# Optimization experiments

Measured on AMD Instinct MI355X. Metric: run time of the kernel, lower is better.

Reference implementation:

```python
import jax, jax.numpy as jnp
import numpy as np
from jax import lax

V, B, T, H = 16, 64, 256, 128  # num_variables, batch, seq_len, rnn_hidden_size
FC, C = 256, 10                # fc_hidden_size, num_classes


def setup_inputs() -> dict:
    key = jax.random.key(0)
    ks = jax.random.split(key, 8)
    s = 1.0 / np.sqrt(H)
    return {
        "x":   jax.random.normal(ks[0], (V, B, T, 1), jnp.float32),
        "Wih": jax.random.uniform(ks[1], (V, 3 * H, 1), jnp.float32, -s, s),
        "Whh": jax.random.uniform(ks[2], (V, 3 * H, H), jnp.float32, -s, s),
        "bih": jnp.zeros((V, 3 * H), jnp.float32),
        "bhh": jnp.zeros((V, 3 * H), jnp.float32),
        "Wp":  jax.random.normal(ks[3], (V, H), jnp.float32) * s,  # xavier-ish
        "bp":  jnp.zeros((V,), jnp.float32),
        "W1":  jax.random.normal(ks[4], (FC, V), jnp.float32) * (1.0 / np.sqrt(V)),
        "b1":  jnp.zeros((FC,), jnp.float32),
        "W2":  jax.random.normal(ks[5], (C, FC), jnp.float32) * (1.0 / np.sqrt(FC)),
        "b2":  jnp.zeros((C,), jnp.float32),
    }


def reference(x, Wih, Whh, bih, bhh, Wp, bp, W1, b1, W2, b2):
    # Batched multi-head GRU: all V independent heads scanned together.
    # Precompute input-side gates for all steps: [T, V, B, 3H]
    gi = jnp.einsum('vbti,vgi->tvbg', x, Wih) + bih[None, :, None, :]

    def step(h, gi_t):
        gh = jnp.einsum('vbh,vgh->vbg', h, Whh) + bhh[:, None, :]
        i_r, i_z, i_n = jnp.split(gi_t, 3, axis=-1)
        h_r, h_z, h_n = jnp.split(gh, 3, axis=-1)
        r = jax.nn.sigmoid(i_r + h_r)
        z = jax.nn.sigmoid(i_z + h_z)
        n = jnp.tanh(i_n + r * h_n)
        h_new = (1.0 - z) * n + z * h  # PyTorch GRU update
        return h_new, None

    h0 = jnp.zeros((x.shape[0], x.shape[1], Whh.shape[-1]), x.dtype)
    h_last, _ = lax.scan(step, h0, gi)  # [V, B, H] — last timestep hidden

    # per-variable Linear(H, 1), then concat over variables -> [B, V]
    concat = jnp.einsum('vbh,vh->bv', h_last, Wp) + bp[None, :]

    # Classifier: Linear -> ReLU -> Linear
    hfc = jax.nn.relu(concat @ W1.T + b1)
    return hfc @ W2.T + b2  # [B, C]
```

## Files before the change

### kernel.cpp

```cpp
#include <hip/hip_runtime.h>

#define NV  16
#define NB  64
#define NT  256
#define NH  128
#define NFC 256
#define NC  10

typedef _Float16 half8  __attribute__((ext_vector_type(8)));
typedef _Float16 half4t __attribute__((ext_vector_type(4)));
typedef float    f32x4  __attribute__((ext_vector_type(4)));

__global__ __launch_bounds__(512, 2) void gru_scan_kernel(
    const float* __restrict__ x,   const float* __restrict__ Wih,
    const float* __restrict__ Whh, const float* __restrict__ bih,
    const float* __restrict__ bhh, const float* __restrict__ Wp,
    const float* __restrict__ bp,  float* __restrict__ concat_ws)
{
    __shared__ __align__(16) _Float16 frag[2][2048];
    __shared__ float xT[NT][17];
    __shared__ float pc[8][16];

    const int tid = threadIdx.x;
    const int w   = tid >> 6;
    const int l   = tid & 63;
    const int r   = l & 15;
    const int m4  = l >> 4;
    const int bid = blockIdx.x;
    const int v   = bid >> 2;
    const int b0  = (bid & 3) << 4;
    const int j0  = (w << 4) + (m4 << 2);

    constexpr float L2E = 1.44269504088896340736f;
    const float SCL0 = -L2E, SCL1 = -L2E, SCL2 = 2.0f * L2E;

    {
        const int rr = tid >> 5;
        const int t0 = (tid & 31) << 3;
        const float* xp = x + ((size_t)(v * NB + b0 + rr) * NT + t0);
        float4 a = *(const float4*)xp;
        float4 b = *(const float4*)(xp + 4);
        xT[t0+0][rr] = a.x; xT[t0+1][rr] = a.y; xT[t0+2][rr] = a.z; xT[t0+3][rr] = a.w;
        xT[t0+4][rr] = b.x; xT[t0+5][rr] = b.y; xT[t0+6][rr] = b.z; xT[t0+7][rr] = b.w;
    }
    ((unsigned long long*)(&frag[0][0]))[tid] = 0ull;

    half8 afr[3][4];
    #pragma unroll
    for (int g = 0; g < 3; ++g) {
        const float s = (g == 2) ? SCL2 : SCL0;
        #pragma unroll
        for (int kb = 0; kb < 4; ++kb) {
            const float* wpp = Whh + (size_t)(v * 384 + g * 128 + (w << 4) + r) * 128
                             + kb * 32 + m4 * 8;
            float4 lo = *(const float4*)wpp;
            float4 hi = *(const float4*)(wpp + 4);
            half8 hf;
            hf[0]=(_Float16)(s*lo.x); hf[1]=(_Float16)(s*lo.y);
            hf[2]=(_Float16)(s*lo.z); hf[3]=(_Float16)(s*lo.w);
            hf[4]=(_Float16)(s*hi.x); hf[5]=(_Float16)(s*hi.y);
            hf[6]=(_Float16)(s*hi.z); hf[7]=(_Float16)(s*hi.w);
            afr[g][kb] = hf;
        }
    }

    float wihs_[3][4], bihs_[3][4];
    f32x4 c0i, c1i, c2i;
    #pragma unroll
    for (int g = 0; g < 3; ++g) {
        const float s = (g == 2) ? SCL2 : SCL0;
        #pragma unroll
        for (int q = 0; q < 4; ++q) {
            const int idx = v * 384 + g * 128 + j0 + q;
            wihs_[g][q] = s * Wih[idx];
            bihs_[g][q] = s * bih[idx];
            const float bs = s * bhh[idx];
            if (g == 0) c0i[q] = bs; else if (g == 1) c1i[q] = bs; else c2i[q] = bs;
        }
    }
    float wpv[4];
    #pragma unroll
    for (int q = 0; q < 4; ++q) wpv[q] = Wp[v * NH + j0 + q];

    float h_old[4] = {0.f, 0.f, 0.f, 0.f};

    const int sub8  = (j0 & 31) >> 3;
    const int fwoff = (j0 >> 5) * 512 + (r + 16 * sub8) * 8 + (j0 & 7);
    const int rdoff = l * 8;

    __syncthreads();

    auto step = [&](const _Float16* __restrict__ fb, _Float16* __restrict__ fwb,
                    const float xr) {
        half8 bfr[4];
        #pragma unroll
        for (int kb = 0; kb < 4; ++kb)
            bfr[kb] = *(const half8*)(fb + kb * 512 + rdoff);

        f32x4 acc0 = __builtin_amdgcn_mfma_f32_16x16x32_f16(afr[0][0], bfr[0], c0i, 0, 0, 0);
        f32x4 acc1 = __builtin_amdgcn_mfma_f32_16x16x32_f16(afr[1][0], bfr[0], c1i, 0, 0, 0);
        f32x4 acc2 = __builtin_amdgcn_mfma_f32_16x16x32_f16(afr[2][0], bfr[0], c2i, 0, 0, 0);
        #pragma unroll
        for (int kb = 1; kb < 4; ++kb) {
            acc0 = __builtin_amdgcn_mfma_f32_16x16x32_f16(afr[0][kb], bfr[kb], acc0, 0, 0, 0);
            acc1 = __builtin_amdgcn_mfma_f32_16x16x32_f16(afr[1][kb], bfr[kb], acc1, 0, 0, 0);
            acc2 = __builtin_amdgcn_mfma_f32_16x16x32_f16(afr[2][kb], bfr[kb], acc2, 0, 0, 0);
        }

        float rg[4], av[4];
        #pragma unroll
        for (int q = 0; q < 4; ++q) {
            const float srs = fmaf(xr, wihs_[0][q], bihs_[0][q]) + acc0[q];
            const float szs = fmaf(xr, wihs_[1][q], bihs_[1][q]) + acc1[q];
            rg[q] = __builtin_amdgcn_rcpf(1.f + __builtin_amdgcn_exp2f(srs));
            av[q] = __builtin_amdgcn_exp2f(szs);
        }
        half4t hv;
        #pragma unroll
        for (int q = 0; q < 4; ++q) {
            const float gns = fmaf(xr, wihs_[2][q], bihs_[2][q]);
            const float ccs = fmaf(rg[q], acc2[q], gns);
            const float b   = __builtin_amdgcn_exp2f(-ccs);
            const float a   = av[q];
            const float h   = h_old[q];
            const float num = fmaf(-a, b, a) + fmaf(h, b, h);
            const float den = (1.f + a) * (1.f + b);
            const float hn  = num * __builtin_amdgcn_rcpf(den);
            h_old[q] = hn;
            hv[q] = (_Float16)hn;
        }
        *(half4t*)(fwb + fwoff) = hv;
        __syncthreads();
    };

    for (int t = 0; t < NT; t += 2) {
        const float xa = xT[t][r];
        const float xb = xT[t + 1][r];
        step(&frag[0][0], &frag[1][0], xa);
        step(&frag[1][0], &frag[0][0], xb);
    }

    float partial = h_old[0]*wpv[0] + h_old[1]*wpv[1] + h_old[2]*wpv[2] + h_old[3]*wpv[3];
    partial += __shfl_xor(partial, 16, 64);
    partial += __shfl_xor(partial, 32, 64);
    if (l < 16) pc[w][l] = partial;
    __syncthreads();
    if (tid < 16) {
        float s = bp[v];
        #pragma unroll
        for (int ww = 0; ww < 8; ++ww) s += pc[ww][tid];
        concat_ws[(b0 + tid) * NV + v] = s;
    }
}

__global__ __launch_bounds__(256, 1) void fc_kernel(
    const float* __restrict__ cws, const float* __restrict__ W1,
    const float* __restrict__ b1,  const float* __restrict__ W2,
    const float* __restrict__ b2,  float* __restrict__ out)
{
    __shared__ float cc[NB][NV + 1];
    __shared__ float hfc[NB][NFC + 1];
    const int tid = threadIdx.x;
    for (int i = tid; i < NB * NV; i += 256) cc[i >> 4][i & 15] = cws[i];
    __syncthreads();

    float w1r[NV];
    #pragma unroll
    for (int q = 0; q < NV; q += 4) {
        float4 t4 = *(const float4*)(W1 + tid * NV + q);
        w1r[q] = t4.x; w1r[q+1] = t4.y; w1r[q+2] = t4.z; w1r[q+3] = t4.w;
    }
    const float bb = b1[tid];
    for (int b = 0; b < NB; ++b) {
        float s = bb;
        #pragma unroll
        for (int q = 0; q < NV; ++q) s = fmaf(cc[b][q], w1r[q], s);
        hfc[b][tid] = fmaxf(s, 0.f);
    }
    __syncthreads();

    for (int idx = tid; idx < NB * NC; idx += 256) {
        const int b = idx / NC, c = idx % NC;
        const float* w2r = W2 + c * NFC;
        float s = b2[c];
        #pragma unroll 4
        for (int f = 0; f < NFC; f += 4) {
            float4 wv = *(const float4*)(w2r + f);
            s = fmaf(hfc[b][f+0], wv.x, s);
            s = fmaf(hfc[b][f+1], wv.y, s);
            s = fmaf(hfc[b][f+2], wv.z, s);
            s = fmaf(hfc[b][f+3], wv.w, s);
        }
        out[idx] = s;
    }
}

extern "C" void kernel_launch(void* const* d_in, const int* in_sizes, int n_in,
                              void* d_out, int out_size, void* d_ws, size_t ws_size,
                              hipStream_t stream) {
    const float* x   = (const float*)d_in[0];
    const float* Wih = (const float*)d_in[1];
    const float* Whh = (const float*)d_in[2];
    const float* bih = (const float*)d_in[3];
    const float* bhh = (const float*)d_in[4];
    const float* Wp  = (const float*)d_in[5];
    const float* bp  = (const float*)d_in[6];
    const float* W1  = (const float*)d_in[7];
    const float* b1  = (const float*)d_in[8];
    const float* W2  = (const float*)d_in[9];
    const float* b2  = (const float*)d_in[10];
    float* out = (float*)d_out;
    float* cws = (float*)d_ws;

    gru_scan_kernel<<<dim3(64), dim3(512), 0, stream>>>(x, Wih, Whh, bih, bhh, Wp, bp, cws);
    fc_kernel<<<dim3(1), dim3(256), 0, stream>>>(cws, W1, b1, W2, b2, out);
}
```

Measured before the change: 240.9 us.

## Split batch into 4-row tiles across 256 blocks with shuffle-based gate redistribution

Each GRU block now handles 4 batch rows instead of 16, so the launch grows from 64 to 256 blocks and uses more compute units for the sequential scan. The MFMA still runs at 16-wide N, so 12 of its 16 columns hold zero padding. Lanes use cross-lane shuffles to pick out their own gate value, so each thread does the elementwise work for one hidden unit instead of four. This shortens the per-step elementwise critical path and spreads the latency-bound recurrence over more CUs. The cost is wasted MFMA throughput and extra shuffles every step.

```diff
diff --git a/kernel.cpp b/kernel.cpp
--- a/kernel.cpp
+++ b/kernel.cpp
@@ -8,7 +8,6 @@
 #define NC  10
 
 typedef _Float16 half8  __attribute__((ext_vector_type(8)));
-typedef _Float16 half4t __attribute__((ext_vector_type(4)));
 typedef float    f32x4  __attribute__((ext_vector_type(4)));
 
 __global__ __launch_bounds__(512, 2) void gru_scan_kernel(
@@ -18,37 +17,41 @@
     const float* __restrict__ bp,  float* __restrict__ concat_ws)
 {
     __shared__ __align__(16) _Float16 frag[2][2048];
-    __shared__ float xT[NT][17];
-    __shared__ float pc[8][16];
+    __shared__ float xT[NT][5];
+    __shared__ float pc[8][4];
 
     const int tid = threadIdx.x;
     const int w   = tid >> 6;
     const int l   = tid & 63;
     const int r   = l & 15;
     const int m4  = l >> 4;
+    const int rb  = r & 3;
+    const int s   = r >> 2;
     const int bid = blockIdx.x;
-    const int v   = bid >> 2;
-    const int b0  = (bid & 3) << 4;
+    const int v   = bid >> 4;
+    const int b0  = (bid & 15) << 2;
     const int j0  = (w << 4) + (m4 << 2);
+    const int j   = j0 + s;
 
     constexpr float L2E = 1.44269504088896340736f;
-    const float SCL0 = -L2E, SCL1 = -L2E, SCL2 = 2.0f * L2E;
+    const float SCL0 = -L2E, SCL2 = 2.0f * L2E;
 
     {
-        const int rr = tid >> 5;
-        const int t0 = (tid & 31) << 3;
-        const float* xp = x + ((size_t)(v * NB + b0 + rr) * NT + t0);
-        float4 a = *(const float4*)xp;
-        float4 b = *(const float4*)(xp + 4);
-        xT[t0+0][rr] = a.x; xT[t0+1][rr] = a.y; xT[t0+2][rr] = a.z; xT[t0+3][rr] = a.w;
-        xT[t0+4][rr] = b.x; xT[t0+5][rr] = b.y; xT[t0+6][rr] = b.z; xT[t0+7][rr] = b.w;
-    }
-    ((unsigned long long*)(&frag[0][0]))[tid] = 0ull;
+        const int rr = tid >> 7;
+        const int t0 = (tid & 127) << 1;
+        const float2 xv = *(const float2*)(x + (size_t)(v * NB + b0 + rr) * NT + t0);
+        xT[t0][rr] = xv.x; xT[t0 + 1][rr] = xv.y;
+    }
+    {
+        unsigned* fz = (unsigned*)frag;
+        #pragma unroll
+        for (int i = 0; i < 4; ++i) fz[tid + i * 512] = 0u;
+    }
 
     half8 afr[3][4];
     #pragma unroll
     for (int g = 0; g < 3; ++g) {
-        const float s = (g == 2) ? SCL2 : SCL0;
+        const float sc = (g == 2) ? SCL2 : SCL0;
         #pragma unroll
         for (int kb = 0; kb < 4; ++kb) {
             const float* wpp = Whh + (size_t)(v * 384 + g * 128 + (w << 4) + r) * 128
@@ -56,36 +59,33 @@
             float4 lo = *(const float4*)wpp;
             float4 hi = *(const float4*)(wpp + 4);
             half8 hf;
-            hf[0]=(_Float16)(s*lo.x); hf[1]=(_Float16)(s*lo.y);
-            hf[2]=(_Float16)(s*lo.z); hf[3]=(_Float16)(s*lo.w);
-            hf[4]=(_Float16)(s*hi.x); hf[5]=(_Float16)(s*hi.y);
-            hf[6]=(_Float16)(s*hi.z); hf[7]=(_Float16)(s*hi.w);
+            hf[0]=(_Float16)(sc*lo.x); hf[1]=(_Float16)(sc*lo.y);
+            hf[2]=(_Float16)(sc*lo.z); hf[3]=(_Float16)(sc*lo.w);
+            hf[4]=(_Float16)(sc*hi.x); hf[5]=(_Float16)(sc*hi.y);
+            hf[6]=(_Float16)(sc*hi.z); hf[7]=(_Float16)(sc*hi.w);
             afr[g][kb] = hf;
         }
     }
 
-    float wihs_[3][4], bihs_[3][4];
     f32x4 c0i, c1i, c2i;
     #pragma unroll
+    for (int q = 0; q < 4; ++q) {
+        c0i[q] = SCL0 * bhh[v * 384 +   0 + j0 + q];
+        c1i[q] = SCL0 * bhh[v * 384 + 128 + j0 + q];
+        c2i[q] = SCL2 * bhh[v * 384 + 256 + j0 + q];
+    }
+    float wihs_[3], bihs_[3];
+    #pragma unroll
     for (int g = 0; g < 3; ++g) {
-        const float s = (g == 2) ? SCL2 : SCL0;
-        #pragma unroll
-        for (int q = 0; q < 4; ++q) {
-            const int idx = v * 384 + g * 128 + j0 + q;
-            wihs_[g][q] = s * Wih[idx];
-            bihs_[g][q] = s * bih[idx];
-            const float bs = s * bhh[idx];
-            if (g == 0) c0i[q] = bs; else if (g == 1) c1i[q] = bs; else c2i[q] = bs;
-        }
-    }
-    float wpv[4];
-    #pragma unroll
-    for (int q = 0; q < 4; ++q) wpv[q] = Wp[v * NH + j0 + q];
-
-    float h_old[4] = {0.f, 0.f, 0.f, 0.f};
-
-    const int sub8  = (j0 & 31) >> 3;
-    const int fwoff = (j0 >> 5) * 512 + (r + 16 * sub8) * 8 + (j0 & 7);
+        const float sc = (g == 2) ? SCL2 : SCL0;
+        wihs_[g] = sc * Wih[v * 384 + g * 128 + j];
+        bihs_[g] = sc * bih[v * 384 + g * 128 + j];
+    }
+    const float wpj = Wp[v * NH + j];
+
+    float h_old = 0.f;
+
+    const int fwoff = (j >> 5) * 512 + (rb + 16 * ((j & 31) >> 3)) * 8 + (j & 7);
     const int rdoff = l * 8;
 
     __syncthreads();
@@ -107,49 +107,54 @@
             acc2 = __builtin_amdgcn_mfma_f32_16x16x32_f16(afr[2][kb], bfr[kb], acc2, 0, 0, 0);
         }
 
-        float rg[4], av[4];
-        #pragma unroll
-        for (int q = 0; q < 4; ++q) {
-            const float srs = fmaf(xr, wihs_[0][q], bihs_[0][q]) + acc0[q];
-            const float szs = fmaf(xr, wihs_[1][q], bihs_[1][q]) + acc1[q];
-            rg[q] = __builtin_amdgcn_rcpf(1.f + __builtin_amdgcn_exp2f(srs));
-            av[q] = __builtin_amdgcn_exp2f(szs);
-        }
-        half4t hv;
-        #pragma unroll
-        for (int q = 0; q < 4; ++q) {
-            const float gns = fmaf(xr, wihs_[2][q], bihs_[2][q]);
-            const float ccs = fmaf(rg[q], acc2[q], gns);
-            const float b   = __builtin_amdgcn_exp2f(-ccs);
-            const float a   = av[q];
-            const float h   = h_old[q];
-            const float num = fmaf(-a, b, a) + fmaf(h, b, h);
-            const float den = (1.f + a) * (1.f + b);
-            const float hn  = num * __builtin_amdgcn_rcpf(den);
-            h_old[q] = hn;
-            hv[q] = (_Float16)hn;
-        }
-        *(half4t*)(fwb + fwoff) = hv;
+        const bool sel1 = (s & 1) != 0, sel2 = (s & 2) != 0;
+        float gv[3];
+        #pragma unroll
+        for (int g = 0; g < 3; ++g) {
+            const f32x4& a4 = (g == 0) ? acc0 : (g == 1) ? acc1 : acc2;
+            const float t4  = __shfl_xor(a4[1], 4, 64);
+            const float t8  = __shfl_xor(a4[2], 8, 64);
+            const float t12 = __shfl_xor(a4[3], 12, 64);
+            const float lo  = sel1 ? t4  : a4[0];
+            const float hi  = sel1 ? t12 : t8;
+            gv[g] = sel2 ? hi : lo;
+        }
+
+        const float srs = fmaf(xr, wihs_[0], bihs_[0]) + gv[0];
+        const float szs = fmaf(xr, wihs_[1], bihs_[1]) + gv[1];
+        const float gns = fmaf(xr, wihs_[2], bihs_[2]);
+        const float rg  = __builtin_amdgcn_rcpf(1.f + __builtin_amdgcn_exp2f(srs));
+        const float a   = __builtin_amdgcn_exp2f(szs);
+        const float ccs = fmaf(rg, gv[2], gns);
+        const float b   = __builtin_amdgcn_exp2f(-ccs);
+        const float h   = h_old;
+        const float num = fmaf(-a, b, a) + fmaf(h, b, h);
+        const float den = (1.f + a) * (1.f + b);
+        const float hn  = num * __builtin_amdgcn_rcpf(den);
+        h_old = hn;
+        fwb[fwoff] = (_Float16)hn;
         __syncthreads();
     };
 
     for (int t = 0; t < NT; t += 2) {
-        const float xa = xT[t][r];
-        const float xb = xT[t + 1][r];
+        const float xa = xT[t][rb];
+        const float xb = xT[t + 1][rb];
         step(&frag[0][0], &frag[1][0], xa);
         step(&frag[1][0], &frag[0][0], xb);
     }
 
-    float partial = h_old[0]*wpv[0] + h_old[1]*wpv[1] + h_old[2]*wpv[2] + h_old[3]*wpv[3];
+    float partial = h_old * wpj;
+    partial += __shfl_xor(partial, 4, 64);
+    partial += __shfl_xor(partial, 8, 64);
     partial += __shfl_xor(partial, 16, 64);
     partial += __shfl_xor(partial, 32, 64);
-    if (l < 16) pc[w][l] = partial;
-    __syncthreads();
-    if (tid < 16) {
-        float s = bp[v];
-        #pragma unroll
-        for (int ww = 0; ww < 8; ++ww) s += pc[ww][tid];
-        concat_ws[(b0 + tid) * NV + v] = s;
+    if (l < 4) pc[w][l] = partial;
+    __syncthreads();
+    if (tid < 4) {
+        float acc = bp[v];
+        #pragma unroll
+        for (int ww = 0; ww < 8; ++ww) acc += pc[ww][tid];
+        concat_ws[(b0 + tid) * NV + v] = acc;
     }
 }
 
@@ -172,26 +177,26 @@
     }
     const float bb = b1[tid];
     for (int b = 0; b < NB; ++b) {
-        float s = bb;
-        #pragma unroll
-        for (int q = 0; q < NV; ++q) s = fmaf(cc[b][q], w1r[q], s);
-        hfc[b][tid] = fmaxf(s, 0.f);
+        float sacc = bb;
+        #pragma unroll
+        for (int q = 0; q < NV; ++q) sacc = fmaf(cc[b][q], w1r[q], sacc);
+        hfc[b][tid] = fmaxf(sacc, 0.f);
     }
     __syncthreads();
 
     for (int idx = tid; idx < NB * NC; idx += 256) {
         const int b = idx / NC, c = idx % NC;
         const float* w2r = W2 + c * NFC;
-        float s = b2[c];
+        float sacc = b2[c];
         #pragma unroll 4
         for (int f = 0; f < NFC; f += 4) {
             float4 wv = *(const float4*)(w2r + f);
-            s = fmaf(hfc[b][f+0], wv.x, s);
-            s = fmaf(hfc[b][f+1], wv.y, s);
-            s = fmaf(hfc[b][f+2], wv.z, s);
-            s = fmaf(hfc[b][f+3], wv.w, s);
-        }
-        out[idx] = s;
+            sacc = fmaf(hfc[b][f+0], wv.x, sacc);
+            sacc = fmaf(hfc[b][f+1], wv.y, sacc);
+            sacc = fmaf(hfc[b][f+2], wv.z, sacc);
+            sacc = fmaf(hfc[b][f+3], wv.w, sacc);
+        }
+        out[idx] = sacc;
     }
 }
 
@@ -212,6 +217,6 @@
     float* out = (float*)d_out;
     float* cws = (float*)d_ws;
 
-    gru_scan_kernel<<<dim3(64), dim3(512), 0, stream>>>(x, Wih, Whh, bih, bhh, Wp, bp, cws);
+    gru_scan_kernel<<<dim3(256), dim3(512), 0, stream>>>(x, Wih, Whh, bih, bhh, Wp, bp, cws);
     fc_kernel<<<dim3(1), dim3(256), 0, stream>>>(cws, W1, b1, W2, b2, out);
 }
```

Result: slower. 263.0 us (+9.2%).
